# Performance work log

Measured on AMD Instinct MI355X. Metric: run time of the kernel, lower is better.

## Reference

```python
import jax, jax.numpy as jnp
import numpy as np

N_P, N_A, N_S = 100000, 150000, 1000
D_IN, N_HID, N_OUT = 256, 256, 64
E_PA, E_PS = 800000, 100000
HOP = 3


def spmm(row, col, val, h, n_rows):
    # sparse A (edge list) @ dense h : gather source rows, scale, scatter-add to dest rows
    return jax.ops.segment_sum(val[:, None] * h[col], row, num_segments=n_rows)


def setup_inputs() -> dict:
    key = jax.random.key(0)
    ks = jax.random.split(key, 30)
    inp = {}
    inp['x_P'] = jax.random.normal(ks[0], (N_P, D_IN), jnp.float32)
    inp['x_A'] = jax.random.normal(ks[1], (N_A, D_IN), jnp.float32)
    inp['x_S'] = jax.random.normal(ks[2], (N_S, D_IN), jnp.float32)
    inp['pa_row'] = jax.random.randint(ks[3], (E_PA,), 0, N_P, jnp.int32)
    inp['pa_col'] = jax.random.randint(ks[4], (E_PA,), 0, N_A, jnp.int32)
    inp['pa_val'] = jax.random.uniform(ks[5], (E_PA,), jnp.float32)
    inp['ps_row'] = jax.random.randint(ks[6], (E_PS,), 0, N_P, jnp.int32)
    inp['ps_col'] = jax.random.randint(ks[7], (E_PS,), 0, N_S, jnp.int32)
    inp['ps_val'] = jax.random.uniform(ks[8], (E_PS,), jnp.float32)
    inp['ap_row'] = jax.random.randint(ks[9], (E_PA,), 0, N_A, jnp.int32)
    inp['ap_col'] = jax.random.randint(ks[10], (E_PA,), 0, N_P, jnp.int32)
    inp['ap_val'] = jax.random.uniform(ks[11], (E_PA,), jnp.float32)
    inp['sp_row'] = jax.random.randint(ks[12], (E_PS,), 0, N_S, jnp.int32)
    inp['sp_col'] = jax.random.randint(ks[13], (E_PS,), 0, N_P, jnp.int32)
    inp['sp_val'] = jax.random.uniform(ks[14], (E_PS,), jnp.float32)
    inp['diag_PA'] = jax.random.uniform(ks[15], (N_P, 1), jnp.float32)
    inp['diag_PS'] = jax.random.uniform(ks[16], (N_P, 1), jnp.float32)
    inp['diag_AP'] = jax.random.uniform(ks[17], (N_A, 1), jnp.float32)
    inp['diag_SP'] = jax.random.uniform(ks[18], (N_S, 1), jnp.float32)
    s1 = 0.05
    inp['W1_P'] = jax.random.normal(ks[19], (D_IN, N_HID), jnp.float32) * s1
    inp['b1_P'] = jnp.zeros((N_HID,), jnp.float32)
    inp['W1_A'] = jax.random.normal(ks[20], (D_IN, N_HID), jnp.float32) * s1
    inp['b1_A'] = jnp.zeros((N_HID,), jnp.float32)
    inp['W1_S'] = jax.random.normal(ks[21], (D_IN, N_HID), jnp.float32) * s1
    inp['b1_S'] = jnp.zeros((N_HID,), jnp.float32)
    inp['W2'] = jax.random.normal(ks[22], (N_HID, N_OUT), jnp.float32) * s1
    inp['b2'] = jnp.zeros((N_OUT,), jnp.float32)
    return inp


def reference(x_P, x_A, x_S,
              pa_row, pa_col, pa_val,
              ps_row, ps_col, ps_val,
              ap_row, ap_col, ap_val,
              sp_row, sp_col, sp_val,
              diag_PA, diag_PS, diag_AP, diag_SP,
              W1_P, b1_P, W1_A, b1_A, W1_S, b1_S, W2, b2):
    # input projections (dropout is identity in eval mode)
    xP = jax.nn.relu(x_P @ W1_P + b1_P)
    xA = jax.nn.relu(x_A @ W1_A + b1_A)
    xS = jax.nn.relu(x_S @ W1_S + b1_S)
    hP, hA, hS = xP, xA, xS
    # hop loop; node types updated sequentially (P, A, S) as in the torch dict loop
    for _ in range(HOP):
        hP = 0.5 * ((spmm(pa_row, pa_col, pa_val, hA, N_P) + diag_PA * xP)
                    + (spmm(ps_row, ps_col, ps_val, hS, N_P) + diag_PS * xP))
        hA = spmm(ap_row, ap_col, ap_val, hP, N_A) + diag_AP * xA
        hS = spmm(sp_row, sp_col, sp_val, hP, N_S) + diag_SP * xS
    # target_node_type = 'P'
    return hP @ W2 + b2
```

## Files before the change

kernel.cpp:

```cpp
#include <hip/hip_runtime.h>
#include <hip/hip_bf16.h>


typedef __attribute__((ext_vector_type(8))) short bf16x8;
typedef __attribute__((ext_vector_type(4))) float f32x4;

__device__ inline unsigned short f2bf(float f) {
    unsigned u = __builtin_bit_cast(unsigned, f);
    u += 0x7FFFu + ((u >> 16) & 1u);
    return (unsigned short)(u >> 16);
}
__device__ inline float bf2f(unsigned short h) {
    unsigned u = ((unsigned)h) << 16;
    return __builtin_bit_cast(float, u);
}

__device__ inline void bar_sync() {
    __builtin_amdgcn_sched_barrier(0);
    asm volatile("s_waitcnt lgkmcnt(0)" ::: "memory");
    __builtin_amdgcn_s_barrier();
    __builtin_amdgcn_sched_barrier(0);
}

__global__ void k_prep_count(const float* __restrict__ W1P, const float* __restrict__ W1A,
                             const float* __restrict__ W1S, const float* __restrict__ W2f,
                             unsigned short* __restrict__ out,
                             const int* __restrict__ pa, const int* __restrict__ ps,
                             const int* __restrict__ ap, const int* __restrict__ sp,
                             int* __restrict__ cnt, int nP, int nA, int ePA, int ePS) {
    int i = blockIdx.x * 256 + threadIdx.x;
    if (i < 3 * 65536) {
        int m = i >> 16;
        int r = i & 65535;
        int j = r & 7, l = (r >> 3) & 63, kk = (r >> 9) & 7, nt = (r >> 12) & 15;
        int col = nt * 16 + (l & 15);
        int k = kk * 32 + ((l >> 4) << 3) + j;
        const float* s = (m == 0) ? W1P : (m == 1) ? W1A : W1S;
        out[i] = f2bf(s[k * 256 + col]);
        return;
    } else if (i < 3 * 65536 + 16384) {
        int r = i - 3 * 65536;
        int j = r & 7, l = (r >> 3) & 63, kk = (r >> 9) & 7, nt = (r >> 12) & 3;
        int col = nt * 16 + (l & 15);
        int k = kk * 32 + ((l >> 4) << 3) + j;
        out[i] = f2bf(W2f[k * 64 + col]);
        return;
    }
    i -= 212992;
    int r, base;
    if (i < 0) return;
    if (i < ePA) { r = pa[i]; base = 0; }
    else if (i < ePA + ePS) { r = ps[i - ePA]; base = nP; }
    else if (i < 2 * ePA + ePS) { r = ap[i - ePA - ePS]; base = 2 * nP; }
    else if (i < 2 * ePA + 2 * ePS) { r = sp[i - 2 * ePA - ePS]; base = 2 * nP + nA; }
    else return;
    atomicAdd(&cnt[base + r], 1);
}

__global__ __launch_bounds__(256)
void k_proj_all(const float* __restrict__ xP, const float* __restrict__ xA,
                const float* __restrict__ xS, const unsigned short* __restrict__ Wpk,
                const float* __restrict__ b1P, const float* __restrict__ b1A,
                const float* __restrict__ b1S,
                unsigned short* __restrict__ yP, unsigned short* __restrict__ yA,
                unsigned short* __restrict__ yS, int nP, int nA, int nS) {
    __shared__ unsigned short xs[32 * 256];
    const int TP = (nP + 31) >> 5, TA = (nA + 31) >> 5, TS = (nS + 31) >> 5;
    const int TT = TP + TA + TS;
    const int tid = threadIdx.x, lane = tid & 63, w = tid >> 6;
    const int l15 = lane & 15, lhi = lane >> 4;
    const unsigned short* W2pk = Wpk + 3 * 65536;

    float4 xr[8];
    int t = blockIdx.x;
    if (t >= TT) return;

    {
        const float* x; int r0, nn;
        if (t < TP) { x = xP; r0 = t << 5; nn = nP; }
        else if (t < TP + TA) { x = xA; r0 = (t - TP) << 5; nn = nA; }
        else { x = xS; r0 = (t - TP - TA) << 5; nn = nS; }
        #pragma unroll
        for (int j = 0; j < 4; ++j) {
            int c = tid + j * 256;
            int row = c >> 5, col = (c & 31) << 3;
            int gr = r0 + row;
            float4 z = make_float4(0, 0, 0, 0);
            xr[2 * j] = z; xr[2 * j + 1] = z;
            if (gr < nn) {
                const float4* p = (const float4*)(x + (size_t)gr * 256 + col);
                xr[2 * j] = p[0]; xr[2 * j + 1] = p[1];
            }
        }
    }
    while (t < TT) {
        const unsigned short* W1; const float* b1; unsigned short* y; int r0, nn;
        if (t < TP) { r0 = t << 5; nn = nP; W1 = Wpk; b1 = b1P; y = yP; }
        else if (t < TP + TA) { r0 = (t - TP) << 5; nn = nA; W1 = Wpk + 65536; b1 = b1A; y = yA; }
        else { r0 = (t - TP - TA) << 5; nn = nS; W1 = Wpk + 2 * 65536; b1 = b1S; y = yS; }

        bar_sync();
        #pragma unroll
        for (int j = 0; j < 4; ++j) {
            int c = tid + j * 256;
            int row = c >> 5, col = (c & 31) << 3;
            float4 f0 = xr[2 * j], f1 = xr[2 * j + 1];
            bf16x8 v;
            v[0] = (short)f2bf(f0.x); v[1] = (short)f2bf(f0.y);
            v[2] = (short)f2bf(f0.z); v[3] = (short)f2bf(f0.w);
            v[4] = (short)f2bf(f1.x); v[5] = (short)f2bf(f1.y);
            v[6] = (short)f2bf(f1.z); v[7] = (short)f2bf(f1.w);
            int byte = row * 512 + ((col * 2) ^ ((row & 7) << 4));
            *(bf16x8*)((char*)xs + byte) = v;
        }
        int tn = t + gridDim.x;
        if (tn < TT) {
            const float* x2; int r02, n2;
            if (tn < TP) { x2 = xP; r02 = tn << 5; n2 = nP; }
            else if (tn < TP + TA) { x2 = xA; r02 = (tn - TP) << 5; n2 = nA; }
            else { x2 = xS; r02 = (tn - TP - TA) << 5; n2 = nS; }
            #pragma unroll
            for (int j = 0; j < 4; ++j) {
                int c = tid + j * 256;
                int row = c >> 5, col = (c & 31) << 3;
                int gr = r02 + row;
                float4 z = make_float4(0, 0, 0, 0), a0 = z, a1 = z;
                if (gr < n2) {
                    const float4* q = (const float4*)(x2 + (size_t)gr * 256 + col);
                    a0 = q[0]; a1 = q[1];
                }
                xr[2 * j] = a0; xr[2 * j + 1] = a1;
            }
        }
        bar_sync();

        f32x4 acc[2][4] = {};
        #pragma unroll
        for (int kk = 0; kk < 8; ++kk) {
            int k = kk * 32 + lhi * 8;
            bf16x8 a[2], b[4];
            #pragma unroll
            for (int m = 0; m < 2; ++m) {
                int row = m * 16 + l15;
                int byte = row * 512 + ((k * 2) ^ ((row & 7) << 4));
                a[m] = *(const bf16x8*)((const char*)xs + byte);
            }
            #pragma unroll
            for (int nq = 0; nq < 4; ++nq)
                b[nq] = *(const bf16x8*)(W1 + ((((w * 4 + nq) * 8 + kk) * 64 + lane) << 3));
            #pragma unroll
            for (int m = 0; m < 2; ++m)
                #pragma unroll
                for (int nq = 0; nq < 4; ++nq)
                    acc[m][nq] = __builtin_amdgcn_mfma_f32_16x16x32_bf16(a[m], b[nq], acc[m][nq], 0, 0, 0);
        }
        bar_sync();

        #pragma unroll
        for (int nq = 0; nq < 4; ++nq) {
            int col = w * 64 + nq * 16 + l15;
            float bias = b1[col];
            #pragma unroll
            for (int m = 0; m < 2; ++m)
                #pragma unroll
                for (int q = 0; q < 4; ++q) {
                    int row = m * 16 + lhi * 4 + q;
                    float vv = acc[m][nq][q] + bias;
                    vv = vv > 0.f ? vv : 0.f;
                    int byte = row * 512 + ((col * 2) ^ ((row & 7) << 4));
                    *(unsigned short*)((char*)xs + byte) = f2bf(vv);
                }
        }
        bar_sync();

        if (w < 2) {
            f32x4 acc2[4] = {};
            #pragma unroll
            for (int kk = 0; kk < 8; ++kk) {
                int k = kk * 32 + lhi * 8;
                int row = w * 16 + l15;
                int byte = row * 512 + ((k * 2) ^ ((row & 7) << 4));
                bf16x8 a = *(const bf16x8*)((const char*)xs + byte);
                #pragma unroll
                for (int nq = 0; nq < 4; ++nq) {
                    bf16x8 b = *(const bf16x8*)(W2pk + (((nq * 8 + kk) * 64 + lane) << 3));
                    acc2[nq] = __builtin_amdgcn_mfma_f32_16x16x32_bf16(a, b, acc2[nq], 0, 0, 0);
                }
            }
            #pragma unroll
            for (int nq = 0; nq < 4; ++nq)
                #pragma unroll
                for (int q = 0; q < 4; ++q) {
                    int row = w * 16 + lhi * 4 + q;
                    int gr = r0 + row;
                    if (gr < nn) y[(size_t)gr * 64 + (nq * 16 + l15)] = f2bf(acc2[nq][q]);
                }
        }
        t = tn;
    }
}

__global__ __launch_bounds__(256)
void k_scan1(const int* __restrict__ cnt, int* __restrict__ off,
             int* __restrict__ bsum, int n) {
    __shared__ int sh[256];
    int tid = threadIdx.x;
    int base = blockIdx.x * 1024 + tid * 4;
    int c[4];
    #pragma unroll
    for (int j = 0; j < 4; ++j) c[j] = (base + j < n) ? cnt[base + j] : 0;
    int s = c[0] + c[1] + c[2] + c[3];
    sh[tid] = s;
    __syncthreads();
    #pragma unroll
    for (int o = 1; o < 256; o <<= 1) {
        int v = (tid >= o) ? sh[tid - o] : 0;
        __syncthreads();
        sh[tid] += v;
        __syncthreads();
    }
    int run = sh[tid] - s;
    #pragma unroll
    for (int j = 0; j < 4; ++j) {
        if (base + j < n) off[base + j] = run;
        run += c[j];
    }
    if (tid == 255) bsum[blockIdx.x] = sh[255];
}

__global__ __launch_bounds__(256)
void k_scan2(int* __restrict__ bsum, int nb) {
    __shared__ int sh[256];
    int tid = threadIdx.x;
    int base = tid * 4;
    int v[4];
    #pragma unroll
    for (int j = 0; j < 4; ++j) v[j] = (base + j < nb) ? bsum[base + j] : 0;
    int s = v[0] + v[1] + v[2] + v[3];
    sh[tid] = s;
    __syncthreads();
    #pragma unroll
    for (int o = 1; o < 256; o <<= 1) {
        int x = (tid >= o) ? sh[tid - o] : 0;
        __syncthreads();
        sh[tid] += x;
        __syncthreads();
    }
    int run = sh[tid] - s;
    #pragma unroll
    for (int j = 0; j < 4; ++j) {
        if (base + j < nb) bsum[base + j] = run;
        run += v[j];
    }
}

__global__ void k_scan3(const int* __restrict__ off0, const int* __restrict__ bsum,
                        int* __restrict__ offPA, int* __restrict__ offPS,
                        int* __restrict__ offAP, int* __restrict__ offSP,
                        int* __restrict__ curPA, int* __restrict__ curPS,
                        int* __restrict__ curAP, int* __restrict__ curSP,
                        int nP, int nA, int nS, int ePA, int ePS) {
    int i = blockIdx.x * 256 + threadIdx.x;
    int NC = 2 * nP + nA + nS;
    if (i >= NC) return;
    int v = off0[i] + bsum[i >> 10];
    int g0, loc, ng, nE; int *og, *cg;
    if (i < nP)                { g0 = 0;           loc = i;                ng = nP; nE = ePA; og = offPA; cg = curPA; }
    else if (i < 2 * nP)       { g0 = nP;          loc = i - nP;           ng = nP; nE = ePS; og = offPS; cg = curPS; }
    else if (i < 2 * nP + nA)  { g0 = 2 * nP;      loc = i - 2 * nP;       ng = nA; nE = ePA; og = offAP; cg = curAP; }
    else                       { g0 = 2 * nP + nA; loc = i - 2 * nP - nA;  ng = nS; nE = ePS; og = offSP; cg = curSP; }
    int basev = off0[g0] + bsum[g0 >> 10];
    int rel = v - basev;
    og[loc] = rel; cg[loc] = rel;
    if (loc == 0) og[ng] = nE;
}

__global__ void k_scatter_all(const int* __restrict__ pa_r, const int* __restrict__ pa_c, const float* __restrict__ pa_v,
                              const int* __restrict__ ps_r, const int* __restrict__ ps_c, const float* __restrict__ ps_v,
                              const int* __restrict__ ap_r, const int* __restrict__ ap_c, const float* __restrict__ ap_v,
                              const int* __restrict__ sp_r, const int* __restrict__ sp_c, const float* __restrict__ sp_v,
                              int* __restrict__ curPA, int* __restrict__ curPS,
                              int* __restrict__ curAP, int* __restrict__ curSP,
                              int2* __restrict__ entPA, int2* __restrict__ entPS,
                              int2* __restrict__ entAP, int2* __restrict__ entSP,
                              int ePA, int ePS) {
    int i = blockIdx.x * 256 + threadIdx.x;
    const int *r, *c; const float* v; int* cur; int2* ent; int e;
    if (i < ePA) { e = i; r = pa_r; c = pa_c; v = pa_v; cur = curPA; ent = entPA; }
    else if (i < ePA + ePS) { e = i - ePA; r = ps_r; c = ps_c; v = ps_v; cur = curPS; ent = entPS; }
    else if (i < 2 * ePA + ePS) { e = i - ePA - ePS; r = ap_r; c = ap_c; v = ap_v; cur = curAP; ent = entAP; }
    else if (i < 2 * ePA + 2 * ePS) { e = i - 2 * ePA - ePS; r = sp_r; c = sp_c; v = sp_v; cur = curSP; ent = entSP; }
    else return;
    int rr = r[e];
    int pp = atomicAdd(&cur[rr], 1);
    ent[pp] = make_int2(c[e], __float_as_int(v[e]));
}

__device__ inline void fma4(float acc[4], float w, uint2 g) {
    acc[0] = fmaf(w, __builtin_bit_cast(float, g.x << 16), acc[0]);
    acc[1] = fmaf(w, __builtin_bit_cast(float, g.x & 0xffff0000u), acc[1]);
    acc[2] = fmaf(w, __builtin_bit_cast(float, g.y << 16), acc[2]);
    acc[3] = fmaf(w, __builtin_bit_cast(float, g.y & 0xffff0000u), acc[3]);
}

template<int TWO>
__device__ inline void quad_gather(const int2* __restrict__ ent, int s, int t,
                                   const unsigned short* __restrict__ src,
                                   int sub, int chunk, float acc[4]) {
    for (int e = s; e < t; e += (TWO ? 8 : 4)) {
        int i0 = e + sub;
        int c0 = i0 < t ? i0 : t - 1;
        int2 E0 = ent[c0];
        float w0 = i0 < t ? __int_as_float(E0.y) : 0.f;
        uint2 g0 = ((const uint2*)(src + ((size_t)(unsigned)E0.x << 6)))[chunk];
        if (TWO) {
            int i1 = e + 4 + sub;
            int c1 = i1 < t ? i1 : t - 1;
            int2 E1 = ent[c1];
            float w1 = i1 < t ? __int_as_float(E1.y) : 0.f;
            uint2 g1 = ((const uint2*)(src + ((size_t)(unsigned)E1.x << 6)))[chunk];
            fma4(acc, w0, g0);
            fma4(acc, w1, g1);
        } else {
            fma4(acc, w0, g0);
        }
    }
}

__global__ __launch_bounds__(256)
void k_rowAS(unsigned short* __restrict__ hA, const unsigned short* __restrict__ yA,
             const float* __restrict__ dAP, const int* __restrict__ offAP,
             const int2* __restrict__ entAP,
             unsigned short* __restrict__ hS, const unsigned short* __restrict__ yS,
             const float* __restrict__ dSP, const int* __restrict__ offSP,
             const int2* __restrict__ entSP,
             const unsigned short* __restrict__ srcP, int nA, int nS) {
    int r = (blockIdx.x * 256 + threadIdx.x) >> 6;
    int lane = threadIdx.x & 63;
    int sub = lane >> 4, chunk = lane & 15;
    const int* off; const int2* ent; const unsigned short* y;
    const float* dg; unsigned short* dst;
    if (r < nA) { off = offAP; ent = entAP; y = yA; dg = dAP; dst = hA; }
    else if ((r -= nA) < nS) { off = offSP; ent = entSP; y = yS; dg = dSP; dst = hS; }
    else return;
    float acc[4] = {0.f, 0.f, 0.f, 0.f};
    int s = off[r], t = off[r + 1];
    float d = dg[r];
    uint2 gy = ((const uint2*)(y + (size_t)r * 64))[chunk];
    quad_gather<1>(ent, s, t, srcP, sub, chunk, acc);
    #pragma unroll
    for (int j = 0; j < 4; ++j) {
        acc[j] += __shfl_xor(acc[j], 16, 64);
        acc[j] += __shfl_xor(acc[j], 32, 64);
    }
    if (sub == 0) {
        float o0 = acc[0] + d * __builtin_bit_cast(float, gy.x << 16);
        float o1 = acc[1] + d * __builtin_bit_cast(float, gy.x & 0xffff0000u);
        float o2 = acc[2] + d * __builtin_bit_cast(float, gy.y << 16);
        float o3 = acc[3] + d * __builtin_bit_cast(float, gy.y & 0xffff0000u);
        uint2 o;
        o.x = (unsigned)f2bf(o0) | ((unsigned)f2bf(o1) << 16);
        o.y = (unsigned)f2bf(o2) | ((unsigned)f2bf(o3) << 16);
        ((uint2*)(dst + (size_t)r * 64))[chunk] = o;
    }
}

template<int FINAL>
__global__ __launch_bounds__(256)
void k_row2(unsigned short* __restrict__ dst, float* __restrict__ dstf,
            const unsigned short* __restrict__ yP,
            const float* __restrict__ dA, const float* __restrict__ dB,
            const int* __restrict__ offA, const int2* __restrict__ entA,
            const unsigned short* __restrict__ srcA,
            const int* __restrict__ offB, const int2* __restrict__ entB,
            const unsigned short* __restrict__ srcB,
            const float* __restrict__ b2, int n) {
    int r = (blockIdx.x * 256 + threadIdx.x) >> 6;
    int lane = threadIdx.x & 63;
    int sub = lane >> 4, chunk = lane & 15;
    if (r >= n) return;
    float acc[4] = {0.f, 0.f, 0.f, 0.f};
    int sA = offA[r], tA = offA[r + 1];
    int sB = offB[r], tB = offB[r + 1];
    float d = dA[r] + dB[r];
    uint2 gy = ((const uint2*)(yP + (size_t)r * 64))[chunk];
    quad_gather<1>(entA, sA, tA, srcA, sub, chunk, acc);
    quad_gather<0>(entB, sB, tB, srcB, sub, chunk, acc);
    #pragma unroll
    for (int j = 0; j < 4; ++j) {
        acc[j] += __shfl_xor(acc[j], 16, 64);
        acc[j] += __shfl_xor(acc[j], 32, 64);
    }
    if (sub == 0) {
        float o0 = 0.5f * (acc[0] + d * __builtin_bit_cast(float, gy.x << 16));
        float o1 = 0.5f * (acc[1] + d * __builtin_bit_cast(float, gy.x & 0xffff0000u));
        float o2 = 0.5f * (acc[2] + d * __builtin_bit_cast(float, gy.y << 16));
        float o3 = 0.5f * (acc[3] + d * __builtin_bit_cast(float, gy.y & 0xffff0000u));
        if (FINAL) {
            float4 bv = ((const float4*)b2)[chunk];
            float4 o = make_float4(o0 + bv.x, o1 + bv.y, o2 + bv.z, o3 + bv.w);
            ((float4*)(dstf + (size_t)r * 64))[chunk] = o;
        } else {
            uint2 o;
            o.x = (unsigned)f2bf(o0) | ((unsigned)f2bf(o1) << 16);
            o.y = (unsigned)f2bf(o2) | ((unsigned)f2bf(o3) << 16);
            ((uint2*)(dst + (size_t)r * 64))[chunk] = o;
        }
    }
}

extern "C" void kernel_launch(void* const* d_in, const int* in_sizes, int n_in,
                              void* d_out, int out_size, void* d_ws, size_t ws_size,
                              hipStream_t stream) {
    const float* x_P = (const float*)d_in[0];
    const float* x_A = (const float*)d_in[1];
    const float* x_S = (const float*)d_in[2];
    const int* pa_row = (const int*)d_in[3];
    const int* pa_col = (const int*)d_in[4];
    const float* pa_val = (const float*)d_in[5];
    const int* ps_row = (const int*)d_in[6];
    const int* ps_col = (const int*)d_in[7];
    const float* ps_val = (const float*)d_in[8];
    const int* ap_row = (const int*)d_in[9];
    const int* ap_col = (const int*)d_in[10];
    const float* ap_val = (const float*)d_in[11];
    const int* sp_row = (const int*)d_in[12];
    const int* sp_col = (const int*)d_in[13];
    const float* sp_val = (const float*)d_in[14];
    const float* diag_PA = (const float*)d_in[15];
    const float* diag_PS = (const float*)d_in[16];
    const float* diag_AP = (const float*)d_in[17];
    const float* diag_SP = (const float*)d_in[18];
    const float* W1_P = (const float*)d_in[19];
    const float* b1_P = (const float*)d_in[20];
    const float* W1_A = (const float*)d_in[21];
    const float* b1_A = (const float*)d_in[22];
    const float* W1_S = (const float*)d_in[23];
    const float* b1_S = (const float*)d_in[24];
    const float* W2  = (const float*)d_in[25];
    const float* b2  = (const float*)d_in[26];

    const int nP = in_sizes[15], nA = in_sizes[17], nS = in_sizes[18];
    const int ePA = in_sizes[3], ePS = in_sizes[6];
    const int NC = 2 * nP + nA + nS;

    char* base = (char*)d_ws;
    size_t cur = 0;
    auto alloc = [&](size_t bytes) -> char* {
        cur = (cur + 255) & ~(size_t)255;
        char* p = base + cur;
        cur += bytes;
        return p;
    };
    unsigned short* yP = (unsigned short*)alloc((size_t)nP * 64 * 2);
    unsigned short* yA = (unsigned short*)alloc((size_t)nA * 64 * 2);
    unsigned short* yS = (unsigned short*)alloc((size_t)nS * 64 * 2);
    unsigned short* hP = (unsigned short*)alloc((size_t)nP * 64 * 2);
    unsigned short* hA = (unsigned short*)alloc((size_t)nA * 64 * 2);
    unsigned short* hS = (unsigned short*)alloc((size_t)nS * 64 * 2);
    unsigned short* Wpk = (unsigned short*)alloc(212992 * 2);
    int* cnt  = (int*)alloc((size_t)NC * 4);
    int* off0 = (int*)alloc((size_t)NC * 4);
    int* offPA = (int*)alloc((size_t)(nP + 1) * 4);
    int* offPS = (int*)alloc((size_t)(nP + 1) * 4);
    int* offAP = (int*)alloc((size_t)(nA + 1) * 4);
    int* offSP = (int*)alloc((size_t)(nS + 1) * 4);
    int* curPA = (int*)alloc((size_t)nP * 4);
    int* curPS = (int*)alloc((size_t)nP * 4);
    int* curAP = (int*)alloc((size_t)nA * 4);
    int* curSP = (int*)alloc((size_t)nS * 4);
    int2* entPA = (int2*)alloc((size_t)ePA * 8);
    int2* entPS = (int2*)alloc((size_t)ePS * 8);
    int2* entAP = (int2*)alloc((size_t)ePA * 8);
    int2* entSP = (int2*)alloc((size_t)ePS * 8);
    int* bsum = (int*)alloc(1024 * 4);
    (void)ws_size;

    hipMemsetAsync(cnt, 0, (size_t)NC * 4, stream);
    const int eTot = 2 * (ePA + ePS);
    k_prep_count<<<(212992 + eTot + 255) / 256, 256, 0, stream>>>(
        W1_P, W1_A, W1_S, W2, Wpk,
        pa_row, ps_row, ap_row, sp_row, cnt, nP, nA, ePA, ePS);
    const int nb = (NC + 1023) / 1024;
    k_scan1<<<nb, 256, 0, stream>>>(cnt, off0, bsum, NC);
    k_scan2<<<1, 256, 0, stream>>>(bsum, nb);
    k_scan3<<<(NC + 255) / 256, 256, 0, stream>>>(off0, bsum, offPA, offPS, offAP, offSP,
                                                  curPA, curPS, curAP, curSP,
                                                  nP, nA, nS, ePA, ePS);
    k_scatter_all<<<(eTot + 255) / 256, 256, 0, stream>>>(
        pa_row, pa_col, pa_val, ps_row, ps_col, ps_val,
        ap_row, ap_col, ap_val, sp_row, sp_col, sp_val,
        curPA, curPS, curAP, curSP, entPA, entPS, entAP, entSP, ePA, ePS);

    k_proj_all<<<1024, 256, 0, stream>>>(x_P, x_A, x_S, Wpk, b1_P, b1_A, b1_S,
                                         yP, yA, yS, nP, nA, nS);

    const int gbP = (nP + 3) / 4, gbAS = (nA + nS + 3) / 4;
    k_row2<0><<<gbP, 256, 0, stream>>>(hP, nullptr, yP, diag_PA, diag_PS,
                                       offPA, entPA, yA, offPS, entPS, yS, b2, nP);
    k_rowAS<<<gbAS, 256, 0, stream>>>(hA, yA, diag_AP, offAP, entAP,
                                      hS, yS, diag_SP, offSP, entSP, hP, nA, nS);
    k_row2<0><<<gbP, 256, 0, stream>>>(hP, nullptr, yP, diag_PA, diag_PS,
                                       offPA, entPA, hA, offPS, entPS, hS, b2, nP);
    k_rowAS<<<gbAS, 256, 0, stream>>>(hA, yA, diag_AP, offAP, entAP,
                                      hS, yS, diag_SP, offSP, entSP, hP, nA, nS);
    k_row2<1><<<gbP, 256, 0, stream>>>(nullptr, (float*)d_out, yP, diag_PA, diag_PS,
                                       offPA, entPA, hA, offPS, entPS, hS, b2, nP);
}
```

Before: 607.4 us.

## Replace block-cooperative projection with independent per-wave 16-row tiles

The persistent 1024-block projection kernel staged a 32-row x tile in shared memory, prefetched the next tile into registers and synchronised four waves with barriers. It is replaced by a kernel in which each wave owns 16 rows, loads x straight from global memory into MFMA operands, computes all 256 hidden columns in 16 accumulators, and uses only a private LDS slice for the second GEMM. This removes barriers and cross-wave coupling and launches one wave per 16-row group. In exchange each wave reads the whole W1 from cache with no reuse across waves, needs more accumulator registers, and gives up the explicit prefetch overlap.

Result: slower. 860.8 us (+41.7%).

```diff
diff --git a/kernel.cpp b/kernel.cpp
--- a/kernel.cpp
+++ b/kernel.cpp
@@ -13,13 +13,6 @@
 __device__ inline float bf2f(unsigned short h) {
     unsigned u = ((unsigned)h) << 16;
     return __builtin_bit_cast(float, u);
-}
-
-__device__ inline void bar_sync() {
-    __builtin_amdgcn_sched_barrier(0);
-    asm volatile("s_waitcnt lgkmcnt(0)" ::: "memory");
-    __builtin_amdgcn_s_barrier();
-    __builtin_amdgcn_sched_barrier(0);
 }
 
 __global__ void k_prep_count(const float* __restrict__ W1P, const float* __restrict__ W1A,
@@ -58,146 +51,80 @@
 }
 
 __global__ __launch_bounds__(256)
-void k_proj_all(const float* __restrict__ xP, const float* __restrict__ xA,
-                const float* __restrict__ xS, const unsigned short* __restrict__ Wpk,
-                const float* __restrict__ b1P, const float* __restrict__ b1A,
-                const float* __restrict__ b1S,
-                unsigned short* __restrict__ yP, unsigned short* __restrict__ yA,
-                unsigned short* __restrict__ yS, int nP, int nA, int nS) {
-    __shared__ unsigned short xs[32 * 256];
-    const int TP = (nP + 31) >> 5, TA = (nA + 31) >> 5, TS = (nS + 31) >> 5;
-    const int TT = TP + TA + TS;
+void k_proj_wave(const float* __restrict__ xP, const float* __restrict__ xA,
+                 const float* __restrict__ xS, const unsigned short* __restrict__ Wpk,
+                 const float* __restrict__ b1P, const float* __restrict__ b1A,
+                 const float* __restrict__ b1S,
+                 unsigned short* __restrict__ yP, unsigned short* __restrict__ yA,
+                 unsigned short* __restrict__ yS, int nP, int nA, int nS) {
+    __shared__ unsigned short hs[4][4096];
     const int tid = threadIdx.x, lane = tid & 63, w = tid >> 6;
     const int l15 = lane & 15, lhi = lane >> 4;
+    const int GP = (nP + 15) >> 4, GA = (nA + 15) >> 4, GS = (nS + 15) >> 4;
+    int g = blockIdx.x * 4 + w;
+    if (g >= GP + GA + GS) return;
+
+    const float* x; const unsigned short* W1; const float* b1; unsigned short* y;
+    int r0, nn;
+    if (g < GP)            { x = xP; W1 = Wpk;             b1 = b1P; y = yP; r0 = g << 4;             nn = nP; }
+    else if (g < GP + GA)  { x = xA; W1 = Wpk + 65536;     b1 = b1A; y = yA; r0 = (g - GP) << 4;      nn = nA; }
+    else                   { x = xS; W1 = Wpk + 2 * 65536; b1 = b1S; y = yS; r0 = (g - GP - GA) << 4; nn = nS; }
     const unsigned short* W2pk = Wpk + 3 * 65536;
-
-    float4 xr[8];
-    int t = blockIdx.x;
-    if (t >= TT) return;
-
-    {
-        const float* x; int r0, nn;
-        if (t < TP) { x = xP; r0 = t << 5; nn = nP; }
-        else if (t < TP + TA) { x = xA; r0 = (t - TP) << 5; nn = nA; }
-        else { x = xS; r0 = (t - TP - TA) << 5; nn = nS; }
+    char* my = (char*)hs[w];
+
+    int rr = r0 + l15; if (rr >= nn) rr = nn - 1;
+    const float* xrow = x + (size_t)rr * 256;
+
+    f32x4 acc[16] = {};
+    #pragma unroll
+    for (int kk = 0; kk < 8; ++kk) {
+        int cb = kk * 32 + lhi * 8;
+        float4 f0 = *(const float4*)(xrow + cb);
+        float4 f1 = *(const float4*)(xrow + cb + 4);
+        bf16x8 a;
+        a[0] = (short)f2bf(f0.x); a[1] = (short)f2bf(f0.y);
+        a[2] = (short)f2bf(f0.z); a[3] = (short)f2bf(f0.w);
+        a[4] = (short)f2bf(f1.x); a[5] = (short)f2bf(f1.y);
+        a[6] = (short)f2bf(f1.z); a[7] = (short)f2bf(f1.w);
         #pragma unroll
-        for (int j = 0; j < 4; ++j) {
-            int c = tid + j * 256;
-            int row = c >> 5, col = (c & 31) << 3;
-            int gr = r0 + row;
-            float4 z = make_float4(0, 0, 0, 0);
-            xr[2 * j] = z; xr[2 * j + 1] = z;
-            if (gr < nn) {
-                const float4* p = (const float4*)(x + (size_t)gr * 256 + col);
-                xr[2 * j] = p[0]; xr[2 * j + 1] = p[1];
-            }
-        }
-    }
-    while (t < TT) {
-        const unsigned short* W1; const float* b1; unsigned short* y; int r0, nn;
-        if (t < TP) { r0 = t << 5; nn = nP; W1 = Wpk; b1 = b1P; y = yP; }
-        else if (t < TP + TA) { r0 = (t - TP) << 5; nn = nA; W1 = Wpk + 65536; b1 = b1A; y = yA; }
-        else { r0 = (t - TP - TA) << 5; nn = nS; W1 = Wpk + 2 * 65536; b1 = b1S; y = yS; }
-
-        bar_sync();
+        for (int nt = 0; nt < 16; ++nt) {
+            bf16x8 b = *(const bf16x8*)(W1 + (((nt * 8 + kk) * 64 + lane) << 3));
+            acc[nt] = __builtin_amdgcn_mfma_f32_16x16x32_bf16(a, b, acc[nt], 0, 0, 0);
+        }
+    }
+
+    #pragma unroll
+    for (int nt = 0; nt < 16; ++nt) {
+        float bias = b1[nt * 16 + l15];
         #pragma unroll
-        for (int j = 0; j < 4; ++j) {
-            int c = tid + j * 256;
-            int row = c >> 5, col = (c & 31) << 3;
-            float4 f0 = xr[2 * j], f1 = xr[2 * j + 1];
-            bf16x8 v;
-            v[0] = (short)f2bf(f0.x); v[1] = (short)f2bf(f0.y);
-            v[2] = (short)f2bf(f0.z); v[3] = (short)f2bf(f0.w);
-            v[4] = (short)f2bf(f1.x); v[5] = (short)f2bf(f1.y);
-            v[6] = (short)f2bf(f1.z); v[7] = (short)f2bf(f1.w);
-            int byte = row * 512 + ((col * 2) ^ ((row & 7) << 4));
-            *(bf16x8*)((char*)xs + byte) = v;
-        }
-        int tn = t + gridDim.x;
-        if (tn < TT) {
-            const float* x2; int r02, n2;
-            if (tn < TP) { x2 = xP; r02 = tn << 5; n2 = nP; }
-            else if (tn < TP + TA) { x2 = xA; r02 = (tn - TP) << 5; n2 = nA; }
-            else { x2 = xS; r02 = (tn - TP - TA) << 5; n2 = nS; }
-            #pragma unroll
-            for (int j = 0; j < 4; ++j) {
-                int c = tid + j * 256;
-                int row = c >> 5, col = (c & 31) << 3;
-                int gr = r02 + row;
-                float4 z = make_float4(0, 0, 0, 0), a0 = z, a1 = z;
-                if (gr < n2) {
-                    const float4* q = (const float4*)(x2 + (size_t)gr * 256 + col);
-                    a0 = q[0]; a1 = q[1];
-                }
-                xr[2 * j] = a0; xr[2 * j + 1] = a1;
-            }
-        }
-        bar_sync();
-
-        f32x4 acc[2][4] = {};
-        #pragma unroll
-        for (int kk = 0; kk < 8; ++kk) {
-            int k = kk * 32 + lhi * 8;
-            bf16x8 a[2], b[4];
-            #pragma unroll
-            for (int m = 0; m < 2; ++m) {
-                int row = m * 16 + l15;
-                int byte = row * 512 + ((k * 2) ^ ((row & 7) << 4));
-                a[m] = *(const bf16x8*)((const char*)xs + byte);
-            }
-            #pragma unroll
-            for (int nq = 0; nq < 4; ++nq)
-                b[nq] = *(const bf16x8*)(W1 + ((((w * 4 + nq) * 8 + kk) * 64 + lane) << 3));
-            #pragma unroll
-            for (int m = 0; m < 2; ++m)
-                #pragma unroll
-                for (int nq = 0; nq < 4; ++nq)
-                    acc[m][nq] = __builtin_amdgcn_mfma_f32_16x16x32_bf16(a[m], b[nq], acc[m][nq], 0, 0, 0);
-        }
-        bar_sync();
-
+        for (int q = 0; q < 4; ++q) {
+            int row = lhi * 4 + q;
+            float v = acc[nt][q] + bias;
+            v = v > 0.f ? v : 0.f;
+            int byte = row * 512 + (((nt * 16 + l15) * 2) ^ ((row & 7) << 4));
+            *(unsigned short*)(my + byte) = f2bf(v);
+        }
+    }
+
+    f32x4 acc2[4] = {};
+    #pragma unroll
+    for (int kk = 0; kk < 8; ++kk) {
+        int k = kk * 32 + lhi * 8;
+        int byte = l15 * 512 + ((k * 2) ^ ((l15 & 7) << 4));
+        bf16x8 a = *(const bf16x8*)(my + byte);
         #pragma unroll
         for (int nq = 0; nq < 4; ++nq) {
-            int col = w * 64 + nq * 16 + l15;
-            float bias = b1[col];
-            #pragma unroll
-            for (int m = 0; m < 2; ++m)
-                #pragma unroll
-                for (int q = 0; q < 4; ++q) {
-                    int row = m * 16 + lhi * 4 + q;
-                    float vv = acc[m][nq][q] + bias;
-                    vv = vv > 0.f ? vv : 0.f;
-                    int byte = row * 512 + ((col * 2) ^ ((row & 7) << 4));
-                    *(unsigned short*)((char*)xs + byte) = f2bf(vv);
-                }
-        }
-        bar_sync();
-
-        if (w < 2) {
-            f32x4 acc2[4] = {};
-            #pragma unroll
-            for (int kk = 0; kk < 8; ++kk) {
-                int k = kk * 32 + lhi * 8;
-                int row = w * 16 + l15;
-                int byte = row * 512 + ((k * 2) ^ ((row & 7) << 4));
-                bf16x8 a = *(const bf16x8*)((const char*)xs + byte);
-                #pragma unroll
-                for (int nq = 0; nq < 4; ++nq) {
-                    bf16x8 b = *(const bf16x8*)(W2pk + (((nq * 8 + kk) * 64 + lane) << 3));
-                    acc2[nq] = __builtin_amdgcn_mfma_f32_16x16x32_bf16(a, b, acc2[nq], 0, 0, 0);
-                }
-            }
-            #pragma unroll
-            for (int nq = 0; nq < 4; ++nq)
-                #pragma unroll
-                for (int q = 0; q < 4; ++q) {
-                    int row = w * 16 + lhi * 4 + q;
-                    int gr = r0 + row;
-                    if (gr < nn) y[(size_t)gr * 64 + (nq * 16 + l15)] = f2bf(acc2[nq][q]);
-                }
-        }
-        t = tn;
-    }
+            bf16x8 b = *(const bf16x8*)(W2pk + (((nq * 8 + kk) * 64 + lane) << 3));
+            acc2[nq] = __builtin_amdgcn_mfma_f32_16x16x32_bf16(a, b, acc2[nq], 0, 0, 0);
+        }
+    }
+    #pragma unroll
+    for (int nq = 0; nq < 4; ++nq)
+        #pragma unroll
+        for (int q = 0; q < 4; ++q) {
+            int r = r0 + lhi * 4 + q;
+            if (r < nn) y[(size_t)r * 64 + nq * 16 + l15] = f2bf(acc2[nq][q]);
+        }
 }
 
 __global__ __launch_bounds__(256)
@@ -492,8 +419,10 @@
         ap_row, ap_col, ap_val, sp_row, sp_col, sp_val,
         curPA, curPS, curAP, curSP, entPA, entPS, entAP, entSP, ePA, ePS);
 
-    k_proj_all<<<1024, 256, 0, stream>>>(x_P, x_A, x_S, Wpk, b1_P, b1_A, b1_S,
-                                         yP, yA, yS, nP, nA, nS);
+    const int GTOT = ((nP + 15) >> 4) + ((nA + 15) >> 4) + ((nS + 15) >> 4);
+    k_proj_wave<<<(GTOT + 3) / 4, 256, 0, stream>>>(x_P, x_A, x_S, Wpk,
+                                                    b1_P, b1_A, b1_S,
+                                                    yP, yA, yS, nP, nA, nS);
 
     const int gbP = (nP + 3) / 4, gbAS = (nA + nS + 3) / 4;
     k_row2<0><<<gbP, 256, 0, stream>>>(hP, nullptr, yP, diag_PA, diag_PS,
```

## Fuse edge scatter into projection kernel, double-buffer LDS, pipeline gathers

Applied to the files above, without the earlier changes.

The CSR edge-scatter work is merged into the projection launch as extra blocks, so the atomic scatter can run concurrently with the MFMA projection instead of as a separate serialized kernel. The projection's shared tile is split into separate input and hidden buffers, which allows two block barriers per tile to be dropped at the cost of twice the LDS use. The row-gather loops are rewritten as a software pipeline that prefetches the next quad of edges while accumulating the current one. In the P-row kernel, the first B-edge load is now issued before the A loop. The pipelined gather keeps fewer loads in flight than the previous two-way unrolled version, so its net effect on memory-latency hiding is uncertain.

Measured after the change: 582.9 us. -4.0%, faster.

```diff
diff --git a/kernel.cpp b/kernel.cpp
--- a/kernel.cpp
+++ b/kernel.cpp
@@ -58,16 +58,42 @@
 }
 
 __global__ __launch_bounds__(256)
-void k_proj_all(const float* __restrict__ xP, const float* __restrict__ xA,
-                const float* __restrict__ xS, const unsigned short* __restrict__ Wpk,
-                const float* __restrict__ b1P, const float* __restrict__ b1A,
-                const float* __restrict__ b1S,
-                unsigned short* __restrict__ yP, unsigned short* __restrict__ yA,
-                unsigned short* __restrict__ yS, int nP, int nA, int nS) {
-    __shared__ unsigned short xs[32 * 256];
+void k_proj_scat(const float* __restrict__ xP, const float* __restrict__ xA,
+                 const float* __restrict__ xS, const unsigned short* __restrict__ Wpk,
+                 const float* __restrict__ b1P, const float* __restrict__ b1A,
+                 const float* __restrict__ b1S,
+                 unsigned short* __restrict__ yP, unsigned short* __restrict__ yA,
+                 unsigned short* __restrict__ yS, int nP, int nA, int nS, int projB,
+                 const int* __restrict__ pa_r, const int* __restrict__ pa_c, const float* __restrict__ pa_v,
+                 const int* __restrict__ ps_r, const int* __restrict__ ps_c, const float* __restrict__ ps_v,
+                 const int* __restrict__ ap_r, const int* __restrict__ ap_c, const float* __restrict__ ap_v,
+                 const int* __restrict__ sp_r, const int* __restrict__ sp_c, const float* __restrict__ sp_v,
+                 int* __restrict__ curPA, int* __restrict__ curPS,
+                 int* __restrict__ curAP, int* __restrict__ curSP,
+                 int2* __restrict__ entPA, int2* __restrict__ entPS,
+                 int2* __restrict__ entAP, int2* __restrict__ entSP,
+                 int ePA, int ePS) {
+    __shared__ unsigned short xsx[32 * 256];
+    __shared__ unsigned short xsh[32 * 256];
+    const int tid = threadIdx.x;
+
+    if (blockIdx.x >= projB) {
+        int i = (blockIdx.x - projB) * 256 + tid;
+        const int *r, *c; const float* v; int* cur; int2* ent; int e;
+        if (i < ePA) { e = i; r = pa_r; c = pa_c; v = pa_v; cur = curPA; ent = entPA; }
+        else if (i < ePA + ePS) { e = i - ePA; r = ps_r; c = ps_c; v = ps_v; cur = curPS; ent = entPS; }
+        else if (i < 2 * ePA + ePS) { e = i - ePA - ePS; r = ap_r; c = ap_c; v = ap_v; cur = curAP; ent = entAP; }
+        else if (i < 2 * ePA + 2 * ePS) { e = i - 2 * ePA - ePS; r = sp_r; c = sp_c; v = sp_v; cur = curSP; ent = entSP; }
+        else return;
+        int rr = r[e];
+        int pp = atomicAdd(&cur[rr], 1);
+        ent[pp] = make_int2(c[e], __float_as_int(v[e]));
+        return;
+    }
+
     const int TP = (nP + 31) >> 5, TA = (nA + 31) >> 5, TS = (nS + 31) >> 5;
     const int TT = TP + TA + TS;
-    const int tid = threadIdx.x, lane = tid & 63, w = tid >> 6;
+    const int lane = tid & 63, w = tid >> 6;
     const int l15 = lane & 15, lhi = lane >> 4;
     const unsigned short* W2pk = Wpk + 3 * 65536;
 
@@ -99,7 +125,6 @@
         else if (t < TP + TA) { r0 = (t - TP) << 5; nn = nA; W1 = Wpk + 65536; b1 = b1A; y = yA; }
         else { r0 = (t - TP - TA) << 5; nn = nS; W1 = Wpk + 2 * 65536; b1 = b1S; y = yS; }
 
-        bar_sync();
         #pragma unroll
         for (int j = 0; j < 4; ++j) {
             int c = tid + j * 256;
@@ -111,9 +136,9 @@
             v[4] = (short)f2bf(f1.x); v[5] = (short)f2bf(f1.y);
             v[6] = (short)f2bf(f1.z); v[7] = (short)f2bf(f1.w);
             int byte = row * 512 + ((col * 2) ^ ((row & 7) << 4));
-            *(bf16x8*)((char*)xs + byte) = v;
-        }
-        int tn = t + gridDim.x;
+            *(bf16x8*)((char*)xsx + byte) = v;
+        }
+        int tn = t + projB;
         if (tn < TT) {
             const float* x2; int r02, n2;
             if (tn < TP) { x2 = xP; r02 = tn << 5; n2 = nP; }
@@ -143,7 +168,7 @@
             for (int m = 0; m < 2; ++m) {
                 int row = m * 16 + l15;
                 int byte = row * 512 + ((k * 2) ^ ((row & 7) << 4));
-                a[m] = *(const bf16x8*)((const char*)xs + byte);
+                a[m] = *(const bf16x8*)((const char*)xsx + byte);
             }
             #pragma unroll
             for (int nq = 0; nq < 4; ++nq)
@@ -154,7 +179,6 @@
                 for (int nq = 0; nq < 4; ++nq)
                     acc[m][nq] = __builtin_amdgcn_mfma_f32_16x16x32_bf16(a[m], b[nq], acc[m][nq], 0, 0, 0);
         }
-        bar_sync();
 
         #pragma unroll
         for (int nq = 0; nq < 4; ++nq) {
@@ -168,7 +192,7 @@
                     float vv = acc[m][nq][q] + bias;
                     vv = vv > 0.f ? vv : 0.f;
                     int byte = row * 512 + ((col * 2) ^ ((row & 7) << 4));
-                    *(unsigned short*)((char*)xs + byte) = f2bf(vv);
+                    *(unsigned short*)((char*)xsh + byte) = f2bf(vv);
                 }
         }
         bar_sync();
@@ -180,7 +204,7 @@
                 int k = kk * 32 + lhi * 8;
                 int row = w * 16 + l15;
                 int byte = row * 512 + ((k * 2) ^ ((row & 7) << 4));
-                bf16x8 a = *(const bf16x8*)((const char*)xs + byte);
+                bf16x8 a = *(const bf16x8*)((const char*)xsh + byte);
                 #pragma unroll
                 for (int nq = 0; nq < 4; ++nq) {
                     bf16x8 b = *(const bf16x8*)(W2pk + (((nq * 8 + kk) * 64 + lane) << 3));
@@ -275,27 +299,6 @@
     if (loc == 0) og[ng] = nE;
 }
 
-__global__ void k_scatter_all(const int* __restrict__ pa_r, const int* __restrict__ pa_c, const float* __restrict__ pa_v,
-                              const int* __restrict__ ps_r, const int* __restrict__ ps_c, const float* __restrict__ ps_v,
-                              const int* __restrict__ ap_r, const int* __restrict__ ap_c, const float* __restrict__ ap_v,
-                              const int* __restrict__ sp_r, const int* __restrict__ sp_c, const float* __restrict__ sp_v,
-                              int* __restrict__ curPA, int* __restrict__ curPS,
-                              int* __restrict__ curAP, int* __restrict__ curSP,
-                              int2* __restrict__ entPA, int2* __restrict__ entPS,
-                              int2* __restrict__ entAP, int2* __restrict__ entSP,
-                              int ePA, int ePS) {
-    int i = blockIdx.x * 256 + threadIdx.x;
-    const int *r, *c; const float* v; int* cur; int2* ent; int e;
-    if (i < ePA) { e = i; r = pa_r; c = pa_c; v = pa_v; cur = curPA; ent = entPA; }
-    else if (i < ePA + ePS) { e = i - ePA; r = ps_r; c = ps_c; v = ps_v; cur = curPS; ent = entPS; }
-    else if (i < 2 * ePA + ePS) { e = i - ePA - ePS; r = ap_r; c = ap_c; v = ap_v; cur = curAP; ent = entAP; }
-    else if (i < 2 * ePA + 2 * ePS) { e = i - 2 * ePA - ePS; r = sp_r; c = sp_c; v = sp_v; cur = curSP; ent = entSP; }
-    else return;
-    int rr = r[e];
-    int pp = atomicAdd(&cur[rr], 1);
-    ent[pp] = make_int2(c[e], __float_as_int(v[e]));
-}
-
 __device__ inline void fma4(float acc[4], float w, uint2 g) {
     acc[0] = fmaf(w, __builtin_bit_cast(float, g.x << 16), acc[0]);
     acc[1] = fmaf(w, __builtin_bit_cast(float, g.x & 0xffff0000u), acc[1]);
@@ -303,26 +306,28 @@
     acc[3] = fmaf(w, __builtin_bit_cast(float, g.y & 0xffff0000u), acc[3]);
 }
 
-template<int TWO>
-__device__ inline void quad_gather(const int2* __restrict__ ent, int s, int t,
-                                   const unsigned short* __restrict__ src,
-                                   int sub, int chunk, float acc[4]) {
-    for (int e = s; e < t; e += (TWO ? 8 : 4)) {
-        int i0 = e + sub;
-        int c0 = i0 < t ? i0 : t - 1;
-        int2 E0 = ent[c0];
-        float w0 = i0 < t ? __int_as_float(E0.y) : 0.f;
-        uint2 g0 = ((const uint2*)(src + ((size_t)(unsigned)E0.x << 6)))[chunk];
-        if (TWO) {
-            int i1 = e + 4 + sub;
+__device__ inline void quad_pipe(const int2* __restrict__ ent, int s, int t,
+                                 const unsigned short* __restrict__ src,
+                                 int sub, int chunk, float acc[4]) {
+    if (s >= t) return;
+    int i0 = s + sub;
+    int c0 = i0 < t ? i0 : t - 1;
+    int2 Ea = ent[c0];
+    float wa = i0 < t ? __int_as_float(Ea.y) : 0.f;
+    uint2 ga = ((const uint2*)(src + ((size_t)(unsigned)Ea.x << 6)))[chunk];
+    for (int e = s; ; ) {
+        int en = e + 4;
+        if (en < t) {
+            int i1 = en + sub;
             int c1 = i1 < t ? i1 : t - 1;
-            int2 E1 = ent[c1];
-            float w1 = i1 < t ? __int_as_float(E1.y) : 0.f;
-            uint2 g1 = ((const uint2*)(src + ((size_t)(unsigned)E1.x << 6)))[chunk];
-            fma4(acc, w0, g0);
-            fma4(acc, w1, g1);
+            int2 Eb = ent[c1];
+            float wb = i1 < t ? __int_as_float(Eb.y) : 0.f;
+            uint2 gb = ((const uint2*)(src + ((size_t)(unsigned)Eb.x << 6)))[chunk];
+            fma4(acc, wa, ga);
+            wa = wb; ga = gb; e = en;
         } else {
-            fma4(acc, w0, g0);
+            fma4(acc, wa, ga);
+            break;
         }
     }
 }
@@ -347,7 +352,7 @@
     int s = off[r], t = off[r + 1];
     float d = dg[r];
     uint2 gy = ((const uint2*)(y + (size_t)r * 64))[chunk];
-    quad_gather<1>(ent, s, t, srcP, sub, chunk, acc);
+    quad_pipe(ent, s, t, srcP, sub, chunk, acc);
     #pragma unroll
     for (int j = 0; j < 4; ++j) {
         acc[j] += __shfl_xor(acc[j], 16, 64);
@@ -384,8 +389,21 @@
     int sB = offB[r], tB = offB[r + 1];
     float d = dA[r] + dB[r];
     uint2 gy = ((const uint2*)(yP + (size_t)r * 64))[chunk];
-    quad_gather<1>(entA, sA, tA, srcA, sub, chunk, acc);
-    quad_gather<0>(entB, sB, tB, srcB, sub, chunk, acc);
+
+    bool hasB = sB < tB;
+    int2 EB; float wB = 0.f; uint2 gB;
+    if (hasB) {
+        int iB = sB + sub;
+        int cB = iB < tB ? iB : tB - 1;
+        EB = entB[cB];
+        wB = iB < tB ? __int_as_float(EB.y) : 0.f;
+        gB = ((const uint2*)(srcB + ((size_t)(unsigned)EB.x << 6)))[chunk];
+    }
+    quad_pipe(entA, sA, tA, srcA, sub, chunk, acc);
+    if (hasB) {
+        fma4(acc, wB, gB);
+        if (sB + 4 < tB) quad_pipe(entB, sB + 4, tB, srcB, sub, chunk, acc);
+    }
     #pragma unroll
     for (int j = 0; j < 4; ++j) {
         acc[j] += __shfl_xor(acc[j], 16, 64);
@@ -487,13 +505,14 @@
     k_scan3<<<(NC + 255) / 256, 256, 0, stream>>>(off0, bsum, offPA, offPS, offAP, offSP,
                                                   curPA, curPS, curAP, curSP,
                                                   nP, nA, nS, ePA, ePS);
-    k_scatter_all<<<(eTot + 255) / 256, 256, 0, stream>>>(
+
+    const int PROJB = 1024;
+    const int SCB = (eTot + 255) / 256;
+    k_proj_scat<<<PROJB + SCB, 256, 0, stream>>>(
+        x_P, x_A, x_S, Wpk, b1_P, b1_A, b1_S, yP, yA, yS, nP, nA, nS, PROJB,
         pa_row, pa_col, pa_val, ps_row, ps_col, ps_val,
         ap_row, ap_col, ap_val, sp_row, sp_col, sp_val,
         curPA, curPS, curAP, curSP, entPA, entPS, entAP, entSP, ePA, ePS);
-
-    k_proj_all<<<1024, 256, 0, stream>>>(x_P, x_A, x_S, Wpk, b1_P, b1_A, b1_S,
-                                         yP, yA, yS, nP, nA, nS);
 
     const int gbP = (nP + 3) / 4, gbAS = (nA + nS + 3) / 4;
     k_row2<0><<<gbP, 256, 0, stream>>>(hP, nullptr, yP, diag_PA, diag_PS,
```

## Widen gather lanes to 16-byte loads with 8 edges per wave and prefetch

Applied to the files above, without the earlier changes.

Each wave now processes 8 edges concurrently with 8 lanes per 64-wide bf16 row, each lane loading a uint4 (8 values) instead of a uint2. The gather loop is software-pipelined: the next edge's entry and source row are loaded before the current one is accumulated. In the P-row kernel, the first B-edge batch is also prefetched before the A loop runs. This aims to raise memory-level parallelism and load width in the latency-bound sparse gathers, at the cost of more registers and an extra shuffle stage in the reduction.

After: 582.0 us. 1.04x faster.

```diff
diff --git a/kernel.cpp b/kernel.cpp
--- a/kernel.cpp
+++ b/kernel.cpp
@@ -10,10 +10,8 @@
     u += 0x7FFFu + ((u >> 16) & 1u);
     return (unsigned short)(u >> 16);
 }
-__device__ inline float bf2f(unsigned short h) {
-    unsigned u = ((unsigned)h) << 16;
-    return __builtin_bit_cast(float, u);
-}
+__device__ inline float bflo(unsigned u) { return __builtin_bit_cast(float, u << 16); }
+__device__ inline float bfhi(unsigned u) { return __builtin_bit_cast(float, u & 0xffff0000u); }
 
 __device__ inline void bar_sync() {
     __builtin_amdgcn_sched_barrier(0);
@@ -296,35 +294,55 @@
     ent[pp] = make_int2(c[e], __float_as_int(v[e]));
 }
 
-__device__ inline void fma4(float acc[4], float w, uint2 g) {
-    acc[0] = fmaf(w, __builtin_bit_cast(float, g.x << 16), acc[0]);
-    acc[1] = fmaf(w, __builtin_bit_cast(float, g.x & 0xffff0000u), acc[1]);
-    acc[2] = fmaf(w, __builtin_bit_cast(float, g.y << 16), acc[2]);
-    acc[3] = fmaf(w, __builtin_bit_cast(float, g.y & 0xffff0000u), acc[3]);
-}
-
-template<int TWO>
-__device__ inline void quad_gather(const int2* __restrict__ ent, int s, int t,
-                                   const unsigned short* __restrict__ src,
-                                   int sub, int chunk, float acc[4]) {
-    for (int e = s; e < t; e += (TWO ? 8 : 4)) {
-        int i0 = e + sub;
-        int c0 = i0 < t ? i0 : t - 1;
-        int2 E0 = ent[c0];
-        float w0 = i0 < t ? __int_as_float(E0.y) : 0.f;
-        uint2 g0 = ((const uint2*)(src + ((size_t)(unsigned)E0.x << 6)))[chunk];
-        if (TWO) {
-            int i1 = e + 4 + sub;
+__device__ inline void fma8(float acc[8], float w, uint4 g) {
+    acc[0] = fmaf(w, bflo(g.x), acc[0]); acc[1] = fmaf(w, bfhi(g.x), acc[1]);
+    acc[2] = fmaf(w, bflo(g.y), acc[2]); acc[3] = fmaf(w, bfhi(g.y), acc[3]);
+    acc[4] = fmaf(w, bflo(g.z), acc[4]); acc[5] = fmaf(w, bfhi(g.z), acc[5]);
+    acc[6] = fmaf(w, bflo(g.w), acc[6]); acc[7] = fmaf(w, bfhi(g.w), acc[7]);
+}
+
+__device__ inline void oct_pipe(const int2* __restrict__ ent, int s, int t,
+                                const unsigned short* __restrict__ src,
+                                int sub, int chunk, float acc[8]) {
+    if (s >= t) return;
+    int i0 = s + sub;
+    int c0 = i0 < t ? i0 : t - 1;
+    int2 Ea = ent[c0];
+    float wa = i0 < t ? __int_as_float(Ea.y) : 0.f;
+    uint4 ga = ((const uint4*)(src + ((size_t)(unsigned)Ea.x << 6)))[chunk];
+    for (int e = s; ; ) {
+        int en = e + 8;
+        if (en < t) {
+            int i1 = en + sub;
             int c1 = i1 < t ? i1 : t - 1;
-            int2 E1 = ent[c1];
-            float w1 = i1 < t ? __int_as_float(E1.y) : 0.f;
-            uint2 g1 = ((const uint2*)(src + ((size_t)(unsigned)E1.x << 6)))[chunk];
-            fma4(acc, w0, g0);
-            fma4(acc, w1, g1);
+            int2 Eb = ent[c1];
+            float wb = i1 < t ? __int_as_float(Eb.y) : 0.f;
+            uint4 gb = ((const uint4*)(src + ((size_t)(unsigned)Eb.x << 6)))[chunk];
+            fma8(acc, wa, ga);
+            wa = wb; ga = gb; e = en;
         } else {
-            fma4(acc, w0, g0);
-        }
-    }
+            fma8(acc, wa, ga);
+            break;
+        }
+    }
+}
+
+__device__ inline void red8(float acc[8]) {
+    #pragma unroll
+    for (int j = 0; j < 8; ++j) {
+        acc[j] += __shfl_xor(acc[j], 8, 64);
+        acc[j] += __shfl_xor(acc[j], 16, 64);
+        acc[j] += __shfl_xor(acc[j], 32, 64);
+    }
+}
+
+__device__ inline uint4 pack8(const float acc[8]) {
+    uint4 o;
+    o.x = (unsigned)f2bf(acc[0]) | ((unsigned)f2bf(acc[1]) << 16);
+    o.y = (unsigned)f2bf(acc[2]) | ((unsigned)f2bf(acc[3]) << 16);
+    o.z = (unsigned)f2bf(acc[4]) | ((unsigned)f2bf(acc[5]) << 16);
+    o.w = (unsigned)f2bf(acc[6]) | ((unsigned)f2bf(acc[7]) << 16);
+    return o;
 }
 
 __global__ __launch_bounds__(256)
@@ -337,31 +355,24 @@
              const unsigned short* __restrict__ srcP, int nA, int nS) {
     int r = (blockIdx.x * 256 + threadIdx.x) >> 6;
     int lane = threadIdx.x & 63;
-    int sub = lane >> 4, chunk = lane & 15;
+    int sub = lane >> 3, chunk = lane & 7;
     const int* off; const int2* ent; const unsigned short* y;
     const float* dg; unsigned short* dst;
     if (r < nA) { off = offAP; ent = entAP; y = yA; dg = dAP; dst = hA; }
     else if ((r -= nA) < nS) { off = offSP; ent = entSP; y = yS; dg = dSP; dst = hS; }
     else return;
-    float acc[4] = {0.f, 0.f, 0.f, 0.f};
+    float acc[8] = {};
     int s = off[r], t = off[r + 1];
     float d = dg[r];
-    uint2 gy = ((const uint2*)(y + (size_t)r * 64))[chunk];
-    quad_gather<1>(ent, s, t, srcP, sub, chunk, acc);
-    #pragma unroll
-    for (int j = 0; j < 4; ++j) {
-        acc[j] += __shfl_xor(acc[j], 16, 64);
-        acc[j] += __shfl_xor(acc[j], 32, 64);
-    }
+    uint4 gy = ((const uint4*)(y + (size_t)r * 64))[chunk];
+    oct_pipe(ent, s, t, srcP, sub, chunk, acc);
+    red8(acc);
     if (sub == 0) {
-        float o0 = acc[0] + d * __builtin_bit_cast(float, gy.x << 16);
-        float o1 = acc[1] + d * __builtin_bit_cast(float, gy.x & 0xffff0000u);
-        float o2 = acc[2] + d * __builtin_bit_cast(float, gy.y << 16);
-        float o3 = acc[3] + d * __builtin_bit_cast(float, gy.y & 0xffff0000u);
-        uint2 o;
-        o.x = (unsigned)f2bf(o0) | ((unsigned)f2bf(o1) << 16);
-        o.y = (unsigned)f2bf(o2) | ((unsigned)f2bf(o3) << 16);
-        ((uint2*)(dst + (size_t)r * 64))[chunk] = o;
+        acc[0] += d * bflo(gy.x); acc[1] += d * bfhi(gy.x);
+        acc[2] += d * bflo(gy.y); acc[3] += d * bfhi(gy.y);
+        acc[4] += d * bflo(gy.z); acc[5] += d * bfhi(gy.z);
+        acc[6] += d * bflo(gy.w); acc[7] += d * bfhi(gy.w);
+        ((uint4*)(dst + (size_t)r * 64))[chunk] = pack8(acc);
     }
 }
 
@@ -377,34 +388,43 @@
             const float* __restrict__ b2, int n) {
     int r = (blockIdx.x * 256 + threadIdx.x) >> 6;
     int lane = threadIdx.x & 63;
-    int sub = lane >> 4, chunk = lane & 15;
+    int sub = lane >> 3, chunk = lane & 7;
     if (r >= n) return;
-    float acc[4] = {0.f, 0.f, 0.f, 0.f};
+    float acc[8] = {};
     int sA = offA[r], tA = offA[r + 1];
     int sB = offB[r], tB = offB[r + 1];
     float d = dA[r] + dB[r];
-    uint2 gy = ((const uint2*)(yP + (size_t)r * 64))[chunk];
-    quad_gather<1>(entA, sA, tA, srcA, sub, chunk, acc);
-    quad_gather<0>(entB, sB, tB, srcB, sub, chunk, acc);
-    #pragma unroll
-    for (int j = 0; j < 4; ++j) {
-        acc[j] += __shfl_xor(acc[j], 16, 64);
-        acc[j] += __shfl_xor(acc[j], 32, 64);
-    }
+    uint4 gy = ((const uint4*)(yP + (size_t)r * 64))[chunk];
+
+    bool hasB = sB < tB;
+    float wB = 0.f; uint4 gB;
+    if (hasB) {
+        int iB = sB + sub;
+        int cB = iB < tB ? iB : tB - 1;
+        int2 EB = entB[cB];
+        wB = iB < tB ? __int_as_float(EB.y) : 0.f;
+        gB = ((const uint4*)(srcB + ((size_t)(unsigned)EB.x << 6)))[chunk];
+    }
+    oct_pipe(entA, sA, tA, srcA, sub, chunk, acc);
+    if (hasB) {
+        fma8(acc, wB, gB);
+        if (sB + 8 < tB) oct_pipe(entB, sB + 8, tB, srcB, sub, chunk, acc);
+    }
+    red8(acc);
     if (sub == 0) {
-        float o0 = 0.5f * (acc[0] + d * __builtin_bit_cast(float, gy.x << 16));
-        float o1 = 0.5f * (acc[1] + d * __builtin_bit_cast(float, gy.x & 0xffff0000u));
-        float o2 = 0.5f * (acc[2] + d * __builtin_bit_cast(float, gy.y << 16));
-        float o3 = 0.5f * (acc[3] + d * __builtin_bit_cast(float, gy.y & 0xffff0000u));
+        acc[0] = 0.5f * (acc[0] + d * bflo(gy.x)); acc[1] = 0.5f * (acc[1] + d * bfhi(gy.x));
+        acc[2] = 0.5f * (acc[2] + d * bflo(gy.y)); acc[3] = 0.5f * (acc[3] + d * bfhi(gy.y));
+        acc[4] = 0.5f * (acc[4] + d * bflo(gy.z)); acc[5] = 0.5f * (acc[5] + d * bfhi(gy.z));
+        acc[6] = 0.5f * (acc[6] + d * bflo(gy.w)); acc[7] = 0.5f * (acc[7] + d * bfhi(gy.w));
         if (FINAL) {
-            float4 bv = ((const float4*)b2)[chunk];
-            float4 o = make_float4(o0 + bv.x, o1 + bv.y, o2 + bv.z, o3 + bv.w);
-            ((float4*)(dstf + (size_t)r * 64))[chunk] = o;
+            float4 b0 = ((const float4*)b2)[chunk * 2];
+            float4 b1v = ((const float4*)b2)[chunk * 2 + 1];
+            float4 o0 = make_float4(acc[0] + b0.x, acc[1] + b0.y, acc[2] + b0.z, acc[3] + b0.w);
+            float4 o1 = make_float4(acc[4] + b1v.x, acc[5] + b1v.y, acc[6] + b1v.z, acc[7] + b1v.w);
+            ((float4*)(dstf + (size_t)r * 64))[chunk * 2] = o0;
+            ((float4*)(dstf + (size_t)r * 64))[chunk * 2 + 1] = o1;
         } else {
-            uint2 o;
-            o.x = (unsigned)f2bf(o0) | ((unsigned)f2bf(o1) << 16);
-            o.y = (unsigned)f2bf(o2) | ((unsigned)f2bf(o3) << 16);
-            ((uint2*)(dst + (size_t)r * 64))[chunk] = o;
+            ((uint4*)(dst + (size_t)r * 64))[chunk] = pack8(acc);
         }
     }
 }
```
